# Optimization experiments

Hardware: AMD Instinct MI355X
Metric: run time of the kernel (lower is better)

Reference implementation:

```python
import jax, jax.numpy as jnp
import numpy as np
import math

SEQ, BATCH, HID, HEADS = 2048, 2, 2048, 16
HEAD_DIM = HID // HEADS
ROPE_BASE = 10000.0


def setup_inputs() -> dict:
    key = jax.random.key(0)
    k1, k2, k3 = jax.random.split(key, 3)
    hidden_states = jax.random.normal(k1, (SEQ, BATCH, HID), dtype=jnp.float32)
    # causal mask: True means masked (gpt2-style attention_mask_func fills with -10000)
    attention_mask = jnp.triu(jnp.ones((SEQ, SEQ), dtype=bool), k=1)[None, None, :, :]
    w_qkv = jax.random.normal(k2, (3 * HID, HID), dtype=jnp.float32) * 0.02
    b_qkv = jnp.zeros((3 * HID,), dtype=jnp.float32)
    w_dense = jax.random.normal(k3, (HID, HID), dtype=jnp.float32) * 0.02
    b_dense = jnp.zeros((HID,), dtype=jnp.float32)
    return {"hidden_states": hidden_states, "attention_mask": attention_mask,
            "w_qkv": w_qkv, "b_qkv": b_qkv, "w_dense": w_dense, "b_dense": b_dense}


def _rotary_cos_sin(seq_len, dim, dtype):
    inv_freq = 1.0 / (ROPE_BASE ** (jnp.arange(0, dim, 2, dtype=jnp.float32) / dim))
    t = jnp.arange(seq_len, dtype=jnp.float32)
    freqs = jnp.einsum("s,d->sd", t, inv_freq)
    emb = jnp.concatenate([freqs, freqs], axis=-1)  # [s, dim]
    # broadcast to [s, 1, 1, dim] over (batch, heads)
    return jnp.cos(emb)[:, None, None, :].astype(dtype), jnp.sin(emb)[:, None, None, :].astype(dtype)


def _rotate_half(x):
    x1, x2 = jnp.split(x, 2, axis=-1)
    return jnp.concatenate([-x2, x1], axis=-1)


def reference(hidden_states, attention_mask, w_qkv, b_qkv, w_dense, b_dense):
    s, b, h = hidden_states.shape
    # QKV projection: [s, b, 3h] -> [s, b, nh, 3*hd] -> split
    mixed = hidden_states @ w_qkv.T + b_qkv
    mixed = mixed.reshape(s, b, HEADS, 3 * HEAD_DIM)
    q, k, v = jnp.split(mixed, 3, axis=-1)  # each [s, b, nh, hd]
    # rotary (rotary_pct == 1 -> full head dim)
    cos, sin = _rotary_cos_sin(s, HEAD_DIM, q.dtype)
    q = q * cos + _rotate_half(q) * sin
    k = k * cos + _rotate_half(k) * sin
    # attention scores [b, nh, s_q, s_k]
    norm_factor = math.sqrt(HEAD_DIM)
    scores = jnp.einsum("sbhd,tbhd->bhst", q, k) / norm_factor
    scores = jnp.where(attention_mask, jnp.asarray(-10000.0, scores.dtype), scores)
    # softmax in fp32
    probs = jax.nn.softmax(scores.astype(jnp.float32), axis=-1).astype(scores.dtype)
    # context [s, b, nh, hd] -> [s, b, h]
    context = jnp.einsum("bhst,tbhd->sbhd", probs, v).reshape(s, b, h)
    # dense with skip_bias_add: bias returned separately
    output = context @ w_dense.T
    return output, b_dense
```

## Files before the change

### kernel.cpp

```cpp
#include <hip/hip_runtime.h>
#include <cstdint>
#include <math.h>


typedef unsigned short u16;
typedef __bf16 bf16x8 __attribute__((ext_vector_type(8)));
typedef float floatx4 __attribute__((ext_vector_type(4)));

#define SEQ 2048
#define BATCH 2
#define HID 2048
#define NH 16
#define HD 128

__device__ __forceinline__ u16 f2bf(float f) {
  union { float f; uint32_t u; } v; v.f = f;
  uint32_t u = v.u;
  return (u16)((u + 0x7FFFu + ((u >> 16) & 1u)) >> 16);
}

__device__ __forceinline__ void st8_bf16(u16* dst, const float* s) {
  uint32_t pk[4];
#pragma unroll
  for (int j = 0; j < 4; j++)
    pk[j] = (uint32_t)f2bf(s[2 * j]) | ((uint32_t)f2bf(s[2 * j + 1]) << 16);
  *(uint4*)dst = make_uint4(pk[0], pk[1], pk[2], pk[3]);
}

__device__ __forceinline__ void gl16(const u16* g, u16* l) {
  __builtin_amdgcn_global_load_lds(
      (const __attribute__((address_space(1))) void*)g,
      (__attribute__((address_space(3))) void*)l, 16, 0, 0);
}

__global__ __launch_bounds__(256) void cvt_inputs(
    const float* __restrict__ W, const float* __restrict__ Hid,
    u16* __restrict__ wb, u16* __restrict__ Ah, u16* __restrict__ wvw) {
  const int blk = blockIdx.x;
  const int c0 = threadIdx.x * 8;
  const float* src;
  u16* dst;
  if (blk < 4096) {
    int dt = blk >> 7, r = blk & 127;
    int srow = (dt < 16) ? ((dt * 3 + 1) * 128 + r) : (((dt - 16) * 3) * 128 + r);
    src = W + (size_t)srow * HID;
    dst = wb + (size_t)blk * HID;
  } else if (blk < 8192) {
    int r = blk - 4096;
    src = Hid + (size_t)r * HID;
    dst = Ah + (size_t)r * HID;
  } else {
    int v = blk - 8192;
    int h = v >> 7, r = v & 127;
    src = W + (size_t)((h * 3 + 2) * 128 + r) * HID;
    dst = wvw + (size_t)v * HID;
  }
  float t[8];
  *(floatx4*)&t[0] = *(const floatx4*)(src + c0);
  *(floatx4*)&t[4] = *(const floatx4*)(src + c0 + 4);
  st8_bf16(dst + c0, t);
}

__global__ __launch_bounds__(256) void cvt_wd(const float* __restrict__ W,
                                              u16* __restrict__ wd) {
  const int r = blockIdx.x;
  const int c0 = threadIdx.x * 8;
  float t[8];
  const float* src = W + (size_t)r * HID;
  *(floatx4*)&t[0] = *(const floatx4*)(src + c0);
  *(floatx4*)&t[4] = *(const floatx4*)(src + c0 + 4);
  st8_bf16(wd + (size_t)r * HID + c0, t);
}

__global__ __launch_bounds__(256, 2) void qkv_qk(
    const u16* __restrict__ Ah, const u16* __restrict__ wb,
    const float* __restrict__ bias, u16* __restrict__ Qw,
    u16* __restrict__ Kw) {
  __shared__ __align__(16) u16 As[128 * 64];
  __shared__ __align__(16) u16 Bs[128 * 64];
  const int tid = threadIdx.x;
  const int wv = tid >> 6, lane = tid & 63;
  const int quad = lane >> 4, l16 = lane & 15;
  const int wt = blockIdx.x;
  const int bm = blockIdx.y;
  const int rowA0 = bm * 128;
  const int wm = (wv >> 1) * 64;
  const int wn = (wv & 1) * 32;
  const int ntoff[4] = {wn, wn + 16, wn + 64, wn + 80};

  const int lrow = wv * 32 + (lane >> 3);
  const int lcol = (lane & 7) * 8;
  const u16* Ag = Ah + (size_t)(rowA0 + lrow) * HID + lcol;
  const u16* Bg = wb + ((size_t)wt * 128 + lrow) * HID + lcol;
  u16* Al = &As[(wv * 32) * 64];
  u16* Bl = &Bs[(wv * 32) * 64];

  floatx4 acc[4][4];
#pragma unroll
  for (int i = 0; i < 4; i++)
#pragma unroll
    for (int j = 0; j < 4; j++) acc[i][j] = (floatx4){0.f, 0.f, 0.f, 0.f};

  for (int kb = 0; kb < HID; kb += 64) {
#pragma unroll
    for (int j = 0; j < 4; j++) {
      gl16(Ag + (size_t)j * 8 * HID + kb, Al + j * 8 * 64);
      gl16(Bg + (size_t)j * 8 * HID + kb, Bl + j * 8 * 64);
    }
    __syncthreads();
#pragma unroll
    for (int ks = 0; ks < 64; ks += 32) {
      bf16x8 af[4], bfr[4];
#pragma unroll
      for (int mi = 0; mi < 4; mi++)
        af[mi] = *(const bf16x8*)&As[(wm + mi * 16 + l16) * 64 + ks + quad * 8];
#pragma unroll
      for (int ni = 0; ni < 4; ni++)
        bfr[ni] = *(const bf16x8*)&Bs[(ntoff[ni] + l16) * 64 + ks + quad * 8];
#pragma unroll
      for (int mi = 0; mi < 4; mi++)
#pragma unroll
        for (int ni = 0; ni < 4; ni++)
          acc[mi][ni] = __builtin_amdgcn_mfma_f32_16x16x32_bf16(
              af[mi], bfr[ni], acc[mi][ni], 0, 0, 0);
    }
    __syncthreads();
  }

  const int seg = (wt < 16) ? 1 : 0;
  const int head = wt & 15;
  u16* dst = seg ? Kw : Qw;
  float bv[4];
#pragma unroll
  for (int ni = 0; ni < 4; ni++)
    bv[ni] = bias[(head * 3 + seg) * 128 + ntoff[ni] + l16];
  const float RC = 0.20762050593045951f;
  const float f0 = exp2f(-(float)(wn + l16) * RC);
  const float f1 = exp2f(-(float)(wn + 16 + l16) * RC);

#pragma unroll
  for (int mi = 0; mi < 4; mi++) {
#pragma unroll
    for (int reg = 0; reg < 4; reg++) {
      int r = rowA0 + wm + mi * 16 + quad * 4 + reg;
      int s = r >> 1, b = r & 1;
      size_t base = ((size_t)(b * NH + head) * SEQ + s) * HD;
      float sv, cv;
      sincosf((float)s * f0, &sv, &cv);
      {
        float lo = acc[mi][0][reg] + bv[0];
        float hi = acc[mi][2][reg] + bv[2];
        dst[base + wn + l16] = f2bf(lo * cv - hi * sv);
        dst[base + wn + l16 + 64] = f2bf(hi * cv + lo * sv);
      }
      sincosf((float)s * f1, &sv, &cv);
      {
        float lo = acc[mi][1][reg] + bv[1];
        float hi = acc[mi][3][reg] + bv[3];
        dst[base + wn + 16 + l16] = f2bf(lo * cv - hi * sv);
        dst[base + wn + 16 + l16 + 64] = f2bf(hi * cv + lo * sv);
      }
    }
  }
}

__global__ __launch_bounds__(256, 2) void qkv_v(
    const u16* __restrict__ Ah, const u16* __restrict__ wvw,
    const float* __restrict__ bias, u16* __restrict__ Vt) {
  __shared__ __align__(16) u16 As[128 * 64];
  __shared__ __align__(16) u16 Bs[128 * 64];
  const int tid = threadIdx.x;
  const int wv = tid >> 6, lane = tid & 63;
  const int quad = lane >> 4, l16 = lane & 15;
  const int head = blockIdx.x;
  const int bm = blockIdx.y;
  const int rowA0 = bm * 128;
  const int wm = (wv >> 1) * 64;
  const int wn = (wv & 1) * 32;
  const int ntoff[4] = {wn, wn + 16, wn + 64, wn + 80};

  const int lrow = wv * 32 + (lane >> 3);
  const int lcol = (lane & 7) * 8;
  const u16* Ag = Ah + (size_t)(rowA0 + lrow) * HID + lcol;
  const u16* Bg = wvw + ((size_t)head * 128 + lrow) * HID + lcol;
  u16* Al = &As[(wv * 32) * 64];
  u16* Bl = &Bs[(wv * 32) * 64];

  floatx4 acc[4][4];
#pragma unroll
  for (int i = 0; i < 4; i++)
#pragma unroll
    for (int j = 0; j < 4; j++) acc[i][j] = (floatx4){0.f, 0.f, 0.f, 0.f};

  for (int kb = 0; kb < HID; kb += 64) {
#pragma unroll
    for (int j = 0; j < 4; j++) {
      gl16(Ag + (size_t)j * 8 * HID + kb, Al + j * 8 * 64);
      gl16(Bg + (size_t)j * 8 * HID + kb, Bl + j * 8 * 64);
    }
    __syncthreads();
#pragma unroll
    for (int ks = 0; ks < 64; ks += 32) {
      bf16x8 af[4], bfr[4];
#pragma unroll
      for (int mi = 0; mi < 4; mi++)
        af[mi] = *(const bf16x8*)&As[(wm + mi * 16 + l16) * 64 + ks + quad * 8];
#pragma unroll
      for (int ni = 0; ni < 4; ni++)
        bfr[ni] = *(const bf16x8*)&Bs[(ntoff[ni] + l16) * 64 + ks + quad * 8];
#pragma unroll
      for (int mi = 0; mi < 4; mi++)
#pragma unroll
        for (int ni = 0; ni < 4; ni++)
          acc[mi][ni] = __builtin_amdgcn_mfma_f32_16x16x32_bf16(
              af[mi], bfr[ni], acc[mi][ni], 0, 0, 0);
    }
    __syncthreads();
  }

  float bv[4];
#pragma unroll
  for (int ni = 0; ni < 4; ni++)
    bv[ni] = bias[(head * 3 + 2) * 128 + ntoff[ni] + l16];
#pragma unroll
  for (int mi = 0; mi < 4; mi++) {
#pragma unroll
    for (int ni = 0; ni < 4; ni++) {
      int d = ntoff[ni] + l16;
#pragma unroll
      for (int reg = 0; reg < 4; reg++) {
        int r = rowA0 + wm + mi * 16 + quad * 4 + reg;
        int s = r >> 1, b = r & 1;
        Vt[((size_t)(b * NH + head) * HD + d) * SEQ + s] =
            f2bf(acc[mi][ni][reg] + bv[ni]);
      }
    }
  }
}

__global__ __launch_bounds__(256, 2) void attn(
    const u16* __restrict__ Qw, const u16* __restrict__ Kw,
    const u16* __restrict__ Vt, u16* __restrict__ ctx) {
  __shared__ __align__(16) u16 Ks[64 * 128];
  __shared__ __align__(16) u16 Vs[128 * 64];
  __shared__ __align__(16) u16 Pl[4 * 32 * 72];

  const int tid = threadIdx.x;
  const int wv = tid >> 6, lane = tid & 63;
  const int quad = lane >> 4, l16 = lane & 15;

  const int lin = blockIdx.y * gridDim.x + blockIdx.x;
  const int xcdsel = lin & 7;
  const int k = lin >> 3;
  const int bh_hi = k >> 4;
  const int x = k & 15;
  const int bh = (bh_hi << 3) | xcdsel;
  const int qt = ((bh_hi >> 1) & 1) ? (15 - x) : x;

  const int b = bh >> 4, h = bh & 15;
  const int sw = qt * 128 + wv * 32;
  const size_t bhoff = (size_t)bh * SEQ * HD;

  bf16x8 qf[2][4];
#pragma unroll
  for (int mi = 0; mi < 2; mi++)
#pragma unroll
    for (int kc = 0; kc < 4; kc++)
      qf[mi][kc] = *(const bf16x8*)&Qw[bhoff +
                                       (size_t)(sw + mi * 16 + l16) * HD +
                                       kc * 32 + quad * 8];

  floatx4 o[2][8];
#pragma unroll
  for (int mi = 0; mi < 2; mi++)
#pragma unroll
    for (int ni = 0; ni < 8; ni++) o[mi][ni] = (floatx4){0.f, 0.f, 0.f, 0.f};
  float mst[2][4], lst[2][4];
#pragma unroll
  for (int mi = 0; mi < 2; mi++)
#pragma unroll
    for (int r = 0; r < 4; r++) { mst[mi][r] = -1e30f; lst[mi][r] = 0.f; }

  const int nt = qt * 2 + 2;
  const float SCL2 = 0.088388347648318447f * 1.442695040888963f;
  const float MSK2 = -10000.0f * 1.442695040888963f;

#define STAGE(tt)                                                              \
  {                                                                            \
    _Pragma("unroll") for (int i = 0; i < 4; i++) {                            \
      int c = i * 256 + tid;                                                   \
      int rk = c >> 4, uk = c & 15;                                            \
      gl16(&Kw[bhoff + (size_t)((tt) * 64 + rk) * HD + (uk ^ (rk & 7)) * 8],   \
           &Ks[(i * 256 + wv * 64) * 8]);                                      \
      int rv_ = c >> 3, uv = c & 7;                                            \
      gl16(&Vt[bhoff + (size_t)rv_ * SEQ + (tt) * 64 + (uv ^ (rv_ & 7)) * 8],  \
           &Vs[(i * 256 + wv * 64) * 8]);                                      \
    }                                                                          \
  }

  for (int t = 0; t < nt; t++) {
    __syncthreads();
    STAGE(t);
    __syncthreads();

    const bool active = (t * 64 <= sw + 31);
    if (active) {
      floatx4 sa[2][4];
#pragma unroll
      for (int mi = 0; mi < 2; mi++)
#pragma unroll
        for (int ni = 0; ni < 4; ni++) sa[mi][ni] = (floatx4){0.f, 0.f, 0.f, 0.f};
      __builtin_amdgcn_s_setprio(1);
#pragma unroll
      for (int kc = 0; kc < 4; kc++) {
        bf16x8 kf[4];
#pragma unroll
        for (int ni = 0; ni < 4; ni++)
          kf[ni] = *(const bf16x8*)&Ks[(ni * 16 + l16) * 128 +
                                       (((kc * 4 + quad) ^ (l16 & 7)) * 8)];
#pragma unroll
        for (int mi = 0; mi < 2; mi++)
#pragma unroll
          for (int ni = 0; ni < 4; ni++)
            sa[mi][ni] = __builtin_amdgcn_mfma_f32_16x16x32_bf16(
                qf[mi][kc], kf[ni], sa[mi][ni], 0, 0, 0);
      }
      __builtin_amdgcn_s_setprio(0);

      float alpha[2][4];
#pragma unroll
      for (int mi = 0; mi < 2; mi++) {
#pragma unroll
        for (int reg = 0; reg < 4; reg++) {
          int sq = sw + mi * 16 + quad * 4 + reg;
          float rv[4];
#pragma unroll
          for (int ni = 0; ni < 4; ni++) {
            int sk = t * 64 + ni * 16 + l16;
            float v = sa[mi][ni][reg] * SCL2;
            if (sk > sq) v = MSK2;
            rv[ni] = v;
          }
          float rmax = fmaxf(fmaxf(rv[0], rv[1]), fmaxf(rv[2], rv[3]));
          rmax = fmaxf(rmax, __shfl_xor(rmax, 1));
          rmax = fmaxf(rmax, __shfl_xor(rmax, 2));
          rmax = fmaxf(rmax, __shfl_xor(rmax, 4));
          rmax = fmaxf(rmax, __shfl_xor(rmax, 8));
          float mn = fmaxf(mst[mi][reg], rmax);
          float al = exp2f(mst[mi][reg] - mn);
          float rs = 0.f;
#pragma unroll
          for (int ni = 0; ni < 4; ni++) {
            float p = exp2f(rv[ni] - mn);
            rs += p;
            Pl[wv * 2304 + (mi * 16 + quad * 4 + reg) * 72 + ni * 16 + l16] =
                f2bf(p);
          }
          rs += __shfl_xor(rs, 1);
          rs += __shfl_xor(rs, 2);
          rs += __shfl_xor(rs, 4);
          rs += __shfl_xor(rs, 8);
          lst[mi][reg] = lst[mi][reg] * al + rs;
          mst[mi][reg] = mn;
          alpha[mi][reg] = al;
        }
      }
#pragma unroll
      for (int mi = 0; mi < 2; mi++)
#pragma unroll
        for (int ni = 0; ni < 8; ni++)
#pragma unroll
          for (int reg = 0; reg < 4; reg++)
            o[mi][ni][reg] *= alpha[mi][reg];

      __builtin_amdgcn_s_setprio(1);
#pragma unroll
      for (int kc = 0; kc < 2; kc++) {
        bf16x8 pf[2];
#pragma unroll
        for (int mi = 0; mi < 2; mi++)
          pf[mi] = *(const bf16x8*)&Pl[wv * 2304 + (mi * 16 + l16) * 72 +
                                       kc * 32 + quad * 8];
#pragma unroll
        for (int ni = 0; ni < 8; ni++) {
          bf16x8 vf = *(const bf16x8*)&Vs[(ni * 16 + l16) * 64 +
                                          (((kc * 4 + quad) ^ (l16 & 7)) * 8)];
#pragma unroll
          for (int mi = 0; mi < 2; mi++)
            o[mi][ni] = __builtin_amdgcn_mfma_f32_16x16x32_bf16(
                pf[mi], vf, o[mi][ni], 0, 0, 0);
        }
      }
      __builtin_amdgcn_s_setprio(0);
    }
  }

#pragma unroll
  for (int mi = 0; mi < 2; mi++) {
#pragma unroll
    for (int reg = 0; reg < 4; reg++) {
      float inv = 1.0f / lst[mi][reg];
      int sq = sw + mi * 16 + quad * 4 + reg;
      size_t rbase = ((size_t)(sq * BATCH + b)) * HID + h * HD;
#pragma unroll
      for (int ni = 0; ni < 8; ni++)
        ctx[rbase + ni * 16 + l16] = f2bf(o[mi][ni][reg] * inv);
    }
  }
#undef STAGE
}

__global__ __launch_bounds__(256, 2) void dense_gemm(
    const u16* __restrict__ A, const u16* __restrict__ Wd,
    float* __restrict__ out) {
  __shared__ __align__(16) u16 As[128 * 64];
  __shared__ __align__(16) u16 Bs[128 * 64];
  const int tid = threadIdx.x;
  const int wv = tid >> 6, lane = tid & 63;
  const int quad = lane >> 4, l16 = lane & 15;
  const int bn = blockIdx.x, bm = blockIdx.y;
  const int rowA0 = bm * 128, rowB0 = bn * 128;
  const int wm = (wv >> 1) * 64;
  const int wn = (wv & 1) * 64;
  const int ntoff[4] = {wn, wn + 16, wn + 32, wn + 48};

  const int lrow = wv * 32 + (lane >> 3);
  const int lcol = (lane & 7) * 8;
  const u16* Ag = A + (size_t)(rowA0 + lrow) * HID + lcol;
  const u16* Bg = Wd + (size_t)(rowB0 + lrow) * HID + lcol;
  u16* Al = &As[(wv * 32) * 64];
  u16* Bl = &Bs[(wv * 32) * 64];

  floatx4 acc[4][4];
#pragma unroll
  for (int i = 0; i < 4; i++)
#pragma unroll
    for (int j = 0; j < 4; j++) acc[i][j] = (floatx4){0.f, 0.f, 0.f, 0.f};

  for (int kb = 0; kb < HID; kb += 64) {
#pragma unroll
    for (int j = 0; j < 4; j++) {
      gl16(Ag + (size_t)j * 8 * HID + kb, Al + j * 8 * 64);
      gl16(Bg + (size_t)j * 8 * HID + kb, Bl + j * 8 * 64);
    }
    __syncthreads();
#pragma unroll
    for (int ks = 0; ks < 64; ks += 32) {
      bf16x8 af[4], bfr[4];
#pragma unroll
      for (int mi = 0; mi < 4; mi++)
        af[mi] = *(const bf16x8*)&As[(wm + mi * 16 + l16) * 64 + ks + quad * 8];
#pragma unroll
      for (int ni = 0; ni < 4; ni++)
        bfr[ni] = *(const bf16x8*)&Bs[(ntoff[ni] + l16) * 64 + ks + quad * 8];
#pragma unroll
      for (int mi = 0; mi < 4; mi++)
#pragma unroll
        for (int ni = 0; ni < 4; ni++)
          acc[mi][ni] = __builtin_amdgcn_mfma_f32_16x16x32_bf16(
              af[mi], bfr[ni], acc[mi][ni], 0, 0, 0);
    }
    __syncthreads();
  }

#pragma unroll
  for (int mi = 0; mi < 4; mi++)
#pragma unroll
    for (int reg = 0; reg < 4; reg++) {
      int r = rowA0 + wm + mi * 16 + quad * 4 + reg;
#pragma unroll
      for (int ni = 0; ni < 4; ni++)
        out[(size_t)r * HID + bn * 128 + ntoff[ni] + l16] = acc[mi][ni][reg];
    }
}

__global__ void copy_bias(const float* __restrict__ bd, float* __restrict__ out) {
  int i = blockIdx.x * 256 + threadIdx.x;
  if (i < HID) out[(size_t)SEQ * BATCH * HID + i] = bd[i];
}

extern "C" void kernel_launch(void* const* d_in, const int* in_sizes, int n_in,
                              void* d_out, int out_size, void* d_ws,
                              size_t ws_size, hipStream_t stream) {
  const float *hidden = nullptr, *w_qkv = nullptr, *b_qkv = nullptr;
  const float *w_dense = nullptr, *b_dense = nullptr;
  for (int i = 0; i < n_in; i++) {
    long s = in_sizes[i];
    if (s == 8388608L) hidden = (const float*)d_in[i];
    else if (s == 12582912L) w_qkv = (const float*)d_in[i];
    else if (s == 6144L) b_qkv = (const float*)d_in[i];
    else if (s == 4194304L) w_dense = (const float*)d_in[i];
    else if (s == 2048L) b_dense = (const float*)d_in[i];
  }
  float* out = (float*)d_out;

  char* ws = (char*)d_ws;
  u16* Qw = (u16*)(ws);
  u16* Kw = (u16*)(ws + 16777216ll);
  u16* Vt = (u16*)(ws + 33554432ll);
  u16* wb = (u16*)(ws + 33554432ll);
  u16* Ah = (u16*)(ws + 50331648ll);
  u16* ctx = (u16*)(ws + 50331648ll);
  u16* wd = (u16*)(ws);
  u16* wvw = (u16*)d_out;

  cvt_inputs<<<dim3(10240), dim3(256), 0, stream>>>(w_qkv, hidden, wb, Ah, wvw);
  qkv_qk<<<dim3(32, 32), dim3(256), 0, stream>>>(Ah, wb, b_qkv, Qw, Kw);
  qkv_v<<<dim3(16, 32), dim3(256), 0, stream>>>(Ah, wvw, b_qkv, Vt);
  attn<<<dim3(16, 32), dim3(256), 0, stream>>>(Qw, Kw, Vt, ctx);
  cvt_wd<<<dim3(2048), dim3(256), 0, stream>>>(w_dense, wd);
  dense_gemm<<<dim3(16, 32), dim3(256), 0, stream>>>(ctx, wd, out);
  copy_bias<<<dim3(8), dim3(256), 0, stream>>>(b_dense, out);
}
```

Baseline: 452.7 us.

## Split attention across eight waves, merge QKV GEMMs, fold bias copy

The attention kernel now runs 512-thread blocks with eight waves, each owning 16 query rows instead of 32. This is meant to raise occupancy and tighten causal skipping, at the cost of less K/V fragment reuse per wave and more LDS reads. The separate Q/K and V projection kernels are merged into one 48-column grid, and the V transpose buffer moves into the output buffer. The bias copy is folded into the input conversion kernel as an extra block, which removes two kernel launches.

```diff
diff --git a/kernel.cpp b/kernel.cpp
--- a/kernel.cpp
+++ b/kernel.cpp
@@ -35,9 +35,16 @@
 
 __global__ __launch_bounds__(256) void cvt_inputs(
     const float* __restrict__ W, const float* __restrict__ Hid,
-    u16* __restrict__ wb, u16* __restrict__ Ah, u16* __restrict__ wvw) {
+    u16* __restrict__ wb, u16* __restrict__ Ah, u16* __restrict__ wvw,
+    const float* __restrict__ bd, float* __restrict__ out) {
   const int blk = blockIdx.x;
   const int c0 = threadIdx.x * 8;
+  if (blk == 10240) {
+#pragma unroll
+    for (int j = 0; j < 8; j++)
+      out[(size_t)SEQ * BATCH * HID + c0 + j] = bd[c0 + j];
+    return;
+  }
   const float* src;
   u16* dst;
   if (blk < 4096) {
@@ -72,16 +79,17 @@
   st8_bf16(wd + (size_t)r * HID + c0, t);
 }
 
-__global__ __launch_bounds__(256, 2) void qkv_qk(
+__global__ __launch_bounds__(256, 2) void qkv(
     const u16* __restrict__ Ah, const u16* __restrict__ wb,
-    const float* __restrict__ bias, u16* __restrict__ Qw,
-    u16* __restrict__ Kw) {
+    const u16* __restrict__ wvw, const float* __restrict__ bias,
+    u16* __restrict__ Qw, u16* __restrict__ Kw, u16* __restrict__ Vt) {
   __shared__ __align__(16) u16 As[128 * 64];
   __shared__ __align__(16) u16 Bs[128 * 64];
   const int tid = threadIdx.x;
   const int wv = tid >> 6, lane = tid & 63;
   const int quad = lane >> 4, l16 = lane & 15;
   const int wt = blockIdx.x;
+  const bool isv = (wt >= 32);
   const int bm = blockIdx.y;
   const int rowA0 = bm * 128;
   const int wm = (wv >> 1) * 64;
@@ -91,7 +99,8 @@
   const int lrow = wv * 32 + (lane >> 3);
   const int lcol = (lane & 7) * 8;
   const u16* Ag = Ah + (size_t)(rowA0 + lrow) * HID + lcol;
-  const u16* Bg = wb + ((size_t)wt * 128 + lrow) * HID + lcol;
+  const u16* Bg = (isv ? wvw + ((size_t)(wt - 32) * 128 + lrow) * HID
+                       : wb + ((size_t)wt * 128 + lrow) * HID) + lcol;
   u16* Al = &As[(wv * 32) * 64];
   u16* Bl = &Bs[(wv * 32) * 64];
 
@@ -127,123 +136,71 @@
     __syncthreads();
   }
 
-  const int seg = (wt < 16) ? 1 : 0;
-  const int head = wt & 15;
-  u16* dst = seg ? Kw : Qw;
-  float bv[4];
-#pragma unroll
-  for (int ni = 0; ni < 4; ni++)
-    bv[ni] = bias[(head * 3 + seg) * 128 + ntoff[ni] + l16];
-  const float RC = 0.20762050593045951f;
-  const float f0 = exp2f(-(float)(wn + l16) * RC);
-  const float f1 = exp2f(-(float)(wn + 16 + l16) * RC);
-
-#pragma unroll
-  for (int mi = 0; mi < 4; mi++) {
-#pragma unroll
-    for (int reg = 0; reg < 4; reg++) {
-      int r = rowA0 + wm + mi * 16 + quad * 4 + reg;
-      int s = r >> 1, b = r & 1;
-      size_t base = ((size_t)(b * NH + head) * SEQ + s) * HD;
-      float sv, cv;
-      sincosf((float)s * f0, &sv, &cv);
-      {
-        float lo = acc[mi][0][reg] + bv[0];
-        float hi = acc[mi][2][reg] + bv[2];
-        dst[base + wn + l16] = f2bf(lo * cv - hi * sv);
-        dst[base + wn + l16 + 64] = f2bf(hi * cv + lo * sv);
-      }
-      sincosf((float)s * f1, &sv, &cv);
-      {
-        float lo = acc[mi][1][reg] + bv[1];
-        float hi = acc[mi][3][reg] + bv[3];
-        dst[base + wn + 16 + l16] = f2bf(lo * cv - hi * sv);
-        dst[base + wn + 16 + l16 + 64] = f2bf(hi * cv + lo * sv);
-      }
-    }
-  }
-}
-
-__global__ __launch_bounds__(256, 2) void qkv_v(
-    const u16* __restrict__ Ah, const u16* __restrict__ wvw,
-    const float* __restrict__ bias, u16* __restrict__ Vt) {
-  __shared__ __align__(16) u16 As[128 * 64];
-  __shared__ __align__(16) u16 Bs[128 * 64];
-  const int tid = threadIdx.x;
-  const int wv = tid >> 6, lane = tid & 63;
-  const int quad = lane >> 4, l16 = lane & 15;
-  const int head = blockIdx.x;
-  const int bm = blockIdx.y;
-  const int rowA0 = bm * 128;
-  const int wm = (wv >> 1) * 64;
-  const int wn = (wv & 1) * 32;
-  const int ntoff[4] = {wn, wn + 16, wn + 64, wn + 80};
-
-  const int lrow = wv * 32 + (lane >> 3);
-  const int lcol = (lane & 7) * 8;
-  const u16* Ag = Ah + (size_t)(rowA0 + lrow) * HID + lcol;
-  const u16* Bg = wvw + ((size_t)head * 128 + lrow) * HID + lcol;
-  u16* Al = &As[(wv * 32) * 64];
-  u16* Bl = &Bs[(wv * 32) * 64];
-
-  floatx4 acc[4][4];
-#pragma unroll
-  for (int i = 0; i < 4; i++)
-#pragma unroll
-    for (int j = 0; j < 4; j++) acc[i][j] = (floatx4){0.f, 0.f, 0.f, 0.f};
-
-  for (int kb = 0; kb < HID; kb += 64) {
-#pragma unroll
-    for (int j = 0; j < 4; j++) {
-      gl16(Ag + (size_t)j * 8 * HID + kb, Al + j * 8 * 64);
-      gl16(Bg + (size_t)j * 8 * HID + kb, Bl + j * 8 * 64);
-    }
-    __syncthreads();
-#pragma unroll
-    for (int ks = 0; ks < 64; ks += 32) {
-      bf16x8 af[4], bfr[4];
-#pragma unroll
-      for (int mi = 0; mi < 4; mi++)
-        af[mi] = *(const bf16x8*)&As[(wm + mi * 16 + l16) * 64 + ks + quad * 8];
-#pragma unroll
-      for (int ni = 0; ni < 4; ni++)
-        bfr[ni] = *(const bf16x8*)&Bs[(ntoff[ni] + l16) * 64 + ks + quad * 8];
-#pragma unroll
-      for (int mi = 0; mi < 4; mi++)
-#pragma unroll
-        for (int ni = 0; ni < 4; ni++)
-          acc[mi][ni] = __builtin_amdgcn_mfma_f32_16x16x32_bf16(
-              af[mi], bfr[ni], acc[mi][ni], 0, 0, 0);
-    }
-    __syncthreads();
-  }
-
-  float bv[4];
-#pragma unroll
-  for (int ni = 0; ni < 4; ni++)
-    bv[ni] = bias[(head * 3 + 2) * 128 + ntoff[ni] + l16];
-#pragma unroll
-  for (int mi = 0; mi < 4; mi++) {
-#pragma unroll
-    for (int ni = 0; ni < 4; ni++) {
-      int d = ntoff[ni] + l16;
+  if (!isv) {
+    const int seg = (wt < 16) ? 1 : 0;
+    const int head = wt & 15;
+    u16* dst = seg ? Kw : Qw;
+    float bv[4];
+#pragma unroll
+    for (int ni = 0; ni < 4; ni++)
+      bv[ni] = bias[(head * 3 + seg) * 128 + ntoff[ni] + l16];
+    const float RC = 0.20762050593045951f;
+    const float f0 = exp2f(-(float)(wn + l16) * RC);
+    const float f1 = exp2f(-(float)(wn + 16 + l16) * RC);
+
+#pragma unroll
+    for (int mi = 0; mi < 4; mi++) {
 #pragma unroll
       for (int reg = 0; reg < 4; reg++) {
         int r = rowA0 + wm + mi * 16 + quad * 4 + reg;
         int s = r >> 1, b = r & 1;
-        Vt[((size_t)(b * NH + head) * HD + d) * SEQ + s] =
-            f2bf(acc[mi][ni][reg] + bv[ni]);
+        size_t base = ((size_t)(b * NH + head) * SEQ + s) * HD;
+        float sv, cv;
+        sincosf((float)s * f0, &sv, &cv);
+        {
+          float lo = acc[mi][0][reg] + bv[0];
+          float hi = acc[mi][2][reg] + bv[2];
+          dst[base + wn + l16] = f2bf(lo * cv - hi * sv);
+          dst[base + wn + l16 + 64] = f2bf(hi * cv + lo * sv);
+        }
+        sincosf((float)s * f1, &sv, &cv);
+        {
+          float lo = acc[mi][1][reg] + bv[1];
+          float hi = acc[mi][3][reg] + bv[3];
+          dst[base + wn + 16 + l16] = f2bf(lo * cv - hi * sv);
+          dst[base + wn + 16 + l16 + 64] = f2bf(hi * cv + lo * sv);
+        }
       }
     }
-  }
-}
-
-__global__ __launch_bounds__(256, 2) void attn(
+  } else {
+    const int head = wt - 32;
+    float bv[4];
+#pragma unroll
+    for (int ni = 0; ni < 4; ni++)
+      bv[ni] = bias[(head * 3 + 2) * 128 + ntoff[ni] + l16];
+#pragma unroll
+    for (int mi = 0; mi < 4; mi++) {
+#pragma unroll
+      for (int ni = 0; ni < 4; ni++) {
+        int d = ntoff[ni] + l16;
+#pragma unroll
+        for (int reg = 0; reg < 4; reg++) {
+          int r = rowA0 + wm + mi * 16 + quad * 4 + reg;
+          int s = r >> 1, b = r & 1;
+          Vt[((size_t)(b * NH + head) * HD + d) * SEQ + s] =
+              f2bf(acc[mi][ni][reg] + bv[ni]);
+        }
+      }
+    }
+  }
+}
+
+__global__ __launch_bounds__(512, 4) void attn(
     const u16* __restrict__ Qw, const u16* __restrict__ Kw,
     const u16* __restrict__ Vt, u16* __restrict__ ctx) {
   __shared__ __align__(16) u16 Ks[64 * 128];
-  __shared__ __align__(16) u16 Vs[128 * 64];
-  __shared__ __align__(16) u16 Pl[4 * 32 * 72];
+  __shared__ __align__(16) u16 Vs[128 * 64 + 2304];
+  __shared__ __align__(16) u16 Pl[8 * 16 * 72];
 
   const int tid = threadIdx.x;
   const int wv = tid >> 6, lane = tid & 63;
@@ -258,28 +215,21 @@
   const int qt = ((bh_hi >> 1) & 1) ? (15 - x) : x;
 
   const int b = bh >> 4, h = bh & 15;
-  const int sw = qt * 128 + wv * 32;
+  const int sw = qt * 128 + wv * 16;
   const size_t bhoff = (size_t)bh * SEQ * HD;
 
-  bf16x8 qf[2][4];
-#pragma unroll
-  for (int mi = 0; mi < 2; mi++)
-#pragma unroll
-    for (int kc = 0; kc < 4; kc++)
-      qf[mi][kc] = *(const bf16x8*)&Qw[bhoff +
-                                       (size_t)(sw + mi * 16 + l16) * HD +
-                                       kc * 32 + quad * 8];
-
-  floatx4 o[2][8];
-#pragma unroll
-  for (int mi = 0; mi < 2; mi++)
-#pragma unroll
-    for (int ni = 0; ni < 8; ni++) o[mi][ni] = (floatx4){0.f, 0.f, 0.f, 0.f};
-  float mst[2][4], lst[2][4];
-#pragma unroll
-  for (int mi = 0; mi < 2; mi++)
-#pragma unroll
-    for (int r = 0; r < 4; r++) { mst[mi][r] = -1e30f; lst[mi][r] = 0.f; }
+  bf16x8 qf[4];
+#pragma unroll
+  for (int kc = 0; kc < 4; kc++)
+    qf[kc] = *(const bf16x8*)&Qw[bhoff + (size_t)(sw + l16) * HD + kc * 32 +
+                                 quad * 8];
+
+  floatx4 o[8];
+#pragma unroll
+  for (int ni = 0; ni < 8; ni++) o[ni] = (floatx4){0.f, 0.f, 0.f, 0.f};
+  float mst[4], lst[4];
+#pragma unroll
+  for (int r = 0; r < 4; r++) { mst[r] = -1e30f; lst[r] = 0.f; }
 
   const int nt = qt * 2 + 2;
   const float SCL2 = 0.088388347648318447f * 1.442695040888963f;
@@ -287,14 +237,14 @@
 
 #define STAGE(tt)                                                              \
   {                                                                            \
-    _Pragma("unroll") for (int i = 0; i < 4; i++) {                            \
-      int c = i * 256 + tid;                                                   \
+    _Pragma("unroll") for (int i = 0; i < 2; i++) {                            \
+      int c = i * 512 + tid;                                                   \
       int rk = c >> 4, uk = c & 15;                                            \
       gl16(&Kw[bhoff + (size_t)((tt) * 64 + rk) * HD + (uk ^ (rk & 7)) * 8],   \
-           &Ks[(i * 256 + wv * 64) * 8]);                                      \
+           &Ks[(i * 512 + wv * 64) * 8]);                                      \
       int rv_ = c >> 3, uv = c & 7;                                            \
       gl16(&Vt[bhoff + (size_t)rv_ * SEQ + (tt) * 64 + (uv ^ (rv_ & 7)) * 8],  \
-           &Vs[(i * 256 + wv * 64) * 8]);                                      \
+           &Vs[(i * 512 + wv * 64) * 8]);                                      \
     }                                                                          \
   }
 
@@ -303,13 +253,11 @@
     STAGE(t);
     __syncthreads();
 
-    const bool active = (t * 64 <= sw + 31);
+    const bool active = (t * 64 <= sw + 15);
     if (active) {
-      floatx4 sa[2][4];
-#pragma unroll
-      for (int mi = 0; mi < 2; mi++)
-#pragma unroll
-        for (int ni = 0; ni < 4; ni++) sa[mi][ni] = (floatx4){0.f, 0.f, 0.f, 0.f};
+      floatx4 sa[4];
+#pragma unroll
+      for (int ni = 0; ni < 4; ni++) sa[ni] = (floatx4){0.f, 0.f, 0.f, 0.f};
       __builtin_amdgcn_s_setprio(1);
 #pragma unroll
       for (int kc = 0; kc < 4; kc++) {
@@ -319,76 +267,63 @@
           kf[ni] = *(const bf16x8*)&Ks[(ni * 16 + l16) * 128 +
                                        (((kc * 4 + quad) ^ (l16 & 7)) * 8)];
 #pragma unroll
-        for (int mi = 0; mi < 2; mi++)
-#pragma unroll
-          for (int ni = 0; ni < 4; ni++)
-            sa[mi][ni] = __builtin_amdgcn_mfma_f32_16x16x32_bf16(
-                qf[mi][kc], kf[ni], sa[mi][ni], 0, 0, 0);
+        for (int ni = 0; ni < 4; ni++)
+          sa[ni] = __builtin_amdgcn_mfma_f32_16x16x32_bf16(qf[kc], kf[ni],
+                                                           sa[ni], 0, 0, 0);
       }
       __builtin_amdgcn_s_setprio(0);
 
-      float alpha[2][4];
-#pragma unroll
-      for (int mi = 0; mi < 2; mi++) {
-#pragma unroll
-        for (int reg = 0; reg < 4; reg++) {
-          int sq = sw + mi * 16 + quad * 4 + reg;
-          float rv[4];
-#pragma unroll
-          for (int ni = 0; ni < 4; ni++) {
-            int sk = t * 64 + ni * 16 + l16;
-            float v = sa[mi][ni][reg] * SCL2;
-            if (sk > sq) v = MSK2;
-            rv[ni] = v;
-          }
-          float rmax = fmaxf(fmaxf(rv[0], rv[1]), fmaxf(rv[2], rv[3]));
-          rmax = fmaxf(rmax, __shfl_xor(rmax, 1));
-          rmax = fmaxf(rmax, __shfl_xor(rmax, 2));
-          rmax = fmaxf(rmax, __shfl_xor(rmax, 4));
-          rmax = fmaxf(rmax, __shfl_xor(rmax, 8));
-          float mn = fmaxf(mst[mi][reg], rmax);
-          float al = exp2f(mst[mi][reg] - mn);
-          float rs = 0.f;
-#pragma unroll
-          for (int ni = 0; ni < 4; ni++) {
-            float p = exp2f(rv[ni] - mn);
-            rs += p;
-            Pl[wv * 2304 + (mi * 16 + quad * 4 + reg) * 72 + ni * 16 + l16] =
-                f2bf(p);
-          }
-          rs += __shfl_xor(rs, 1);
-          rs += __shfl_xor(rs, 2);
-          rs += __shfl_xor(rs, 4);
-          rs += __shfl_xor(rs, 8);
-          lst[mi][reg] = lst[mi][reg] * al + rs;
-          mst[mi][reg] = mn;
-          alpha[mi][reg] = al;
-        }
+      float alpha[4];
+#pragma unroll
+      for (int reg = 0; reg < 4; reg++) {
+        const int rr = quad * 4 + reg;
+        const int sq = sw + rr;
+        float rv[4];
+#pragma unroll
+        for (int ni = 0; ni < 4; ni++) {
+          int sk = t * 64 + ni * 16 + l16;
+          float v = sa[ni][reg] * SCL2;
+          if (sk > sq) v = MSK2;
+          rv[ni] = v;
+        }
+        float rmax = fmaxf(fmaxf(rv[0], rv[1]), fmaxf(rv[2], rv[3]));
+        rmax = fmaxf(rmax, __shfl_xor(rmax, 1));
+        rmax = fmaxf(rmax, __shfl_xor(rmax, 2));
+        rmax = fmaxf(rmax, __shfl_xor(rmax, 4));
+        rmax = fmaxf(rmax, __shfl_xor(rmax, 8));
+        float mn = fmaxf(mst[reg], rmax);
+        float al = exp2f(mst[reg] - mn);
+        float rs = 0.f;
+#pragma unroll
+        for (int ni = 0; ni < 4; ni++) {
+          float p = exp2f(rv[ni] - mn);
+          rs += p;
+          Pl[wv * 1152 + rr * 72 + ni * 16 + l16] = f2bf(p);
+        }
+        rs += __shfl_xor(rs, 1);
+        rs += __shfl_xor(rs, 2);
+        rs += __shfl_xor(rs, 4);
+        rs += __shfl_xor(rs, 8);
+        lst[reg] = lst[reg] * al + rs;
+        mst[reg] = mn;
+        alpha[reg] = al;
       }
 #pragma unroll
-      for (int mi = 0; mi < 2; mi++)
-#pragma unroll
-        for (int ni = 0; ni < 8; ni++)
-#pragma unroll
-          for (int reg = 0; reg < 4; reg++)
-            o[mi][ni][reg] *= alpha[mi][reg];
+      for (int ni = 0; ni < 8; ni++)
+#pragma unroll
+        for (int reg = 0; reg < 4; reg++) o[ni][reg] *= alpha[reg];
 
       __builtin_amdgcn_s_setprio(1);
 #pragma unroll
       for (int kc = 0; kc < 2; kc++) {
-        bf16x8 pf[2];
-#pragma unroll
-        for (int mi = 0; mi < 2; mi++)
-          pf[mi] = *(const bf16x8*)&Pl[wv * 2304 + (mi * 16 + l16) * 72 +
-                                       kc * 32 + quad * 8];
+        bf16x8 pf =
+            *(const bf16x8*)&Pl[wv * 1152 + l16 * 72 + kc * 32 + quad * 8];
 #pragma unroll
         for (int ni = 0; ni < 8; ni++) {
           bf16x8 vf = *(const bf16x8*)&Vs[(ni * 16 + l16) * 64 +
                                           (((kc * 4 + quad) ^ (l16 & 7)) * 8)];
-#pragma unroll
-          for (int mi = 0; mi < 2; mi++)
-            o[mi][ni] = __builtin_amdgcn_mfma_f32_16x16x32_bf16(
-                pf[mi], vf, o[mi][ni], 0, 0, 0);
+          o[ni] = __builtin_amdgcn_mfma_f32_16x16x32_bf16(pf, vf, o[ni], 0, 0,
+                                                          0);
         }
       }
       __builtin_amdgcn_s_setprio(0);
@@ -396,16 +331,13 @@
   }
 
 #pragma unroll
-  for (int mi = 0; mi < 2; mi++) {
-#pragma unroll
-    for (int reg = 0; reg < 4; reg++) {
-      float inv = 1.0f / lst[mi][reg];
-      int sq = sw + mi * 16 + quad * 4 + reg;
-      size_t rbase = ((size_t)(sq * BATCH + b)) * HID + h * HD;
-#pragma unroll
-      for (int ni = 0; ni < 8; ni++)
-        ctx[rbase + ni * 16 + l16] = f2bf(o[mi][ni][reg] * inv);
-    }
+  for (int reg = 0; reg < 4; reg++) {
+    float inv = 1.0f / lst[reg];
+    int sq = sw + quad * 4 + reg;
+    size_t rbase = ((size_t)(sq * BATCH + b)) * HID + h * HD;
+#pragma unroll
+    for (int ni = 0; ni < 8; ni++)
+      ctx[rbase + ni * 16 + l16] = f2bf(o[ni][reg] * inv);
   }
 #undef STAGE
 }
@@ -474,11 +406,6 @@
     }
 }
 
-__global__ void copy_bias(const float* __restrict__ bd, float* __restrict__ out) {
-  int i = blockIdx.x * 256 + threadIdx.x;
-  if (i < HID) out[(size_t)SEQ * BATCH * HID + i] = bd[i];
-}
-
 extern "C" void kernel_launch(void* const* d_in, const int* in_sizes, int n_in,
                               void* d_out, int out_size, void* d_ws,
                               size_t ws_size, hipStream_t stream) {
@@ -497,18 +424,17 @@
   char* ws = (char*)d_ws;
   u16* Qw = (u16*)(ws);
   u16* Kw = (u16*)(ws + 16777216ll);
-  u16* Vt = (u16*)(ws + 33554432ll);
   u16* wb = (u16*)(ws + 33554432ll);
   u16* Ah = (u16*)(ws + 50331648ll);
   u16* ctx = (u16*)(ws + 50331648ll);
   u16* wd = (u16*)(ws);
   u16* wvw = (u16*)d_out;
-
-  cvt_inputs<<<dim3(10240), dim3(256), 0, stream>>>(w_qkv, hidden, wb, Ah, wvw);
-  qkv_qk<<<dim3(32, 32), dim3(256), 0, stream>>>(Ah, wb, b_qkv, Qw, Kw);
-  qkv_v<<<dim3(16, 32), dim3(256), 0, stream>>>(Ah, wvw, b_qkv, Vt);
-  attn<<<dim3(16, 32), dim3(256), 0, stream>>>(Qw, Kw, Vt, ctx);
+  u16* Vt = (u16*)d_out + 4194304;
+
+  cvt_inputs<<<dim3(10241), dim3(256), 0, stream>>>(w_qkv, hidden, wb, Ah, wvw,
+                                                    b_dense, out);
+  qkv<<<dim3(48, 32), dim3(256), 0, stream>>>(Ah, wb, wvw, b_qkv, Qw, Kw, Vt);
+  attn<<<dim3(16, 32), dim3(512), 0, stream>>>(Qw, Kw, Vt, ctx);
   cvt_wd<<<dim3(2048), dim3(256), 0, stream>>>(w_dense, wd);
   dense_gemm<<<dim3(16, 32), dim3(256), 0, stream>>>(ctx, wd, out);
-  copy_bias<<<dim3(8), dim3(256), 0, stream>>>(b_dense, out);
-}
+}
```

Result: faster. 422.1 us (-6.7%).
